# Performance work log

Hardware: AMD Instinct MI355X
Metric: run time of the kernel (lower is better)

The kernel has to match this reference:

```python
import jax, jax.numpy as jnp
import numpy as np

B, S, H, D = 4, 4096, 1024, 64  # batch, seq, hidden_size, kvq_size


def setup_inputs() -> dict:
    key = jax.random.key(0)
    kx, kk, kq, kv = jax.random.split(key, 4)
    scale = 1.0 / np.sqrt(H)  # torch Linear default init range ~ U(-1/sqrt(in), 1/sqrt(in))
    return {
        "x": jax.random.normal(kx, (B, S, H), dtype=jnp.float32),
        "Wk": jax.random.uniform(kk, (H, D), dtype=jnp.float32, minval=-scale, maxval=scale),
        "Wq": jax.random.uniform(kq, (H, D), dtype=jnp.float32, minval=-scale, maxval=scale),
        "Wv": jax.random.uniform(kv, (H, D), dtype=jnp.float32, minval=-scale, maxval=scale),
    }


def reference(x, Wk, Wq, Wv):
    # Projections: [B,S,H] @ [H,D] -> [B,S,D]
    k = jnp.einsum("bsh,hd->bsd", x, Wk)
    q = jnp.einsum("bsh,hd->bsd", x, Wq)
    v = jnp.einsum("bsh,hd->bsd", x, Wv)
    inv_sqrt_d = 1.0 / jnp.sqrt(jnp.asarray(D, dtype=x.dtype))
    # No softmax: attention = Q K^T / sqrt(D), then @ V
    attn = jnp.einsum("bqd,bkd->bqk", q, k) * inv_sqrt_d  # [B,S,S]
    return jnp.einsum("bqk,bkd->bqd", attn, v)  # [B,S,D]
```

## Files before the change

### kernel.cpp

```cpp
#include <hip/hip_runtime.h>
#include <hip/hip_bf16.h>

#define B_ 4
#define S_ 4096
#define H_ 1024
#define D_ 64
#define BK 64
#define KSTEPS (H_ / BK)

typedef short bf16x8 __attribute__((ext_vector_type(8)));
typedef float f32x4 __attribute__((ext_vector_type(4)));

__device__ inline unsigned short f2bf(float f) {
    union { float f; unsigned u; } v; v.f = f;
    return (unsigned short)((v.u + 0x7fffu + ((v.u >> 16) & 1u)) >> 16);
}
__device__ inline float bf2f(unsigned short u) {
    union { unsigned u; float f; } v; v.u = (unsigned)u << 16;
    return v.f;
}
__device__ inline bf16x8 cvt8(const float4& a, const float4& b) {
    bf16x8 r;
    r[0] = (short)f2bf(a.x); r[1] = (short)f2bf(a.y);
    r[2] = (short)f2bf(a.z); r[3] = (short)f2bf(a.w);
    r[4] = (short)f2bf(b.x); r[5] = (short)f2bf(b.y);
    r[6] = (short)f2bf(b.z); r[7] = (short)f2bf(b.w);
    return r;
}

__global__ void prep_w3(const float* __restrict__ Wk, const float* __restrict__ Wv,
                        const float* __restrict__ Wq, unsigned short* __restrict__ WT) {
    int gid = blockIdx.x * 256 + threadIdx.x;
    int d = gid >> 10;
    int h = gid & (H_ - 1);
    WT[gid]           = f2bf(Wk[h * D_ + d]);
    WT[65536 + gid]   = f2bf(Wv[h * D_ + d]);
    WT[131072 + gid]  = f2bf(Wq[h * D_ + d]);
}

__global__ __launch_bounds__(768)
void kv_moment10(const float* __restrict__ x, const unsigned short* __restrict__ WT,
                 unsigned short* __restrict__ pMb, unsigned short* __restrict__ Qb) {
    int blk = blockIdx.x;
    int b = blk >> 6;
    int c = blk & 63;
    int s0 = c * 64;
    int tid = threadIdx.x;
    int w = tid >> 6, lane = tid & 63;
    int r = lane & 15, kg = lane >> 4;
    int sv = w & 3, pj = w >> 2;

    __shared__ __align__(16) unsigned short L[32768];

    int strow = tid >> 3, sts = tid & 7;
    int sf_st = sts ^ (strow & 7);
    int ws0 = tid * 2, ws1 = tid * 2 + 1;
    int wpj0 = ws0 >> 9, wpj1 = ws1 >> 9;
    int wp0 = ws0 & 511, wp1 = ws1 & 511;
    int wrow0 = wp0 >> 3, wst0 = wp0 & 7, wsf0 = wst0 ^ (wrow0 & 7);
    int wrow1 = wp1 >> 3, wst1 = wp1 & 7, wsf1 = wst1 ^ (wrow1 & 7);

    const float* xbase = x + ((size_t)b * S_ + s0) * H_;

    float4 xr0, xr1;
    bf16x8 wr0, wr1;

#define LOADX(KS) do { if (tid < 512) {                                       \
        const float* src = xbase + (size_t)strow * H_ + (KS) * BK + sts * 8;  \
        xr0 = *(const float4*)(src);                                          \
        xr1 = *(const float4*)(src + 4); } } while (0)
#define LOADW(KS) do {                                                        \
        wr0 = *(const bf16x8*)(WT + wpj0 * 65536 + wrow0 * H_ + (KS) * BK + wst0 * 8); \
        wr1 = *(const bf16x8*)(WT + wpj1 * 65536 + wrow1 * H_ + (KS) * BK + wst1 * 8); \
    } while (0)
#define WRITE(BUF) do {                                                       \
        if (tid < 512)                                                        \
            *(bf16x8*)&L[(BUF) * 4096 + strow * 64 + sf_st * 8] = cvt8(xr0, xr1); \
        *(bf16x8*)&L[8192 + (wpj0 * 2 + (BUF)) * 4096 + wrow0 * 64 + wsf0 * 8] = wr0; \
        *(bf16x8*)&L[8192 + (wpj1 * 2 + (BUF)) * 4096 + wrow1 * 64 + wsf1 * 8] = wr1; \
    } while (0)

    LOADX(0); LOADW(0);
    WRITE(0);
    LOADX(1); LOADW(1);
    __syncthreads();

    f32x4 acc[4] = {};
    int arow_off = (sv * 16 + r) * 64;

    for (int ks = 0; ks < KSTEPS; ++ks) {
        int cur = ks & 1;
        if (ks < KSTEPS - 1) WRITE(cur ^ 1);
        if (ks < KSTEPS - 2) { LOADX(ks + 2); LOADW(ks + 2); }
#pragma unroll
        for (int kc = 0; kc < 2; ++kc) {
            int slot = kc * 4 + kg;
            int sf = (slot ^ (r & 7)) * 8;
            bf16x8 af = *(const bf16x8*)&L[cur * 4096 + arow_off + sf];
#pragma unroll
            for (int nt = 0; nt < 4; ++nt) {
                bf16x8 bw = *(const bf16x8*)&L[8192 + (pj * 2 + cur) * 4096 + (nt * 16 + r) * 64 + sf];
                acc[nt] = __builtin_amdgcn_mfma_f32_16x16x32_bf16(af, bw, acc[nt], 0, 0, 0);
            }
        }
        __syncthreads();
    }

    if (pj < 2) {
#pragma unroll
        for (int nt = 0; nt < 4; ++nt)
#pragma unroll
            for (int i = 0; i < 4; ++i)
                L[pj * 4096 + (sv * 16 + kg * 4 + i) * 64 + nt * 16 + r] = f2bf(acc[nt][i]);
    }
    __syncthreads();
    if (pj == 2) {
        unsigned short* qrow = Qb + ((size_t)b * S_ + s0 + sv * 16) * 64;
#pragma unroll
        for (int nt = 0; nt < 4; ++nt)
#pragma unroll
            for (int i = 0; i < 4; ++i)
                qrow[(kg * 4 + i) * 64 + nt * 16 + r] = f2bf(acc[nt][i]);
    } else if (w < 8) {
        int et = w & 3, dh2 = w >> 2;
        f32x4 accM[2] = {};
#pragma unroll
        for (int ks2 = 0; ks2 < 2; ++ks2) {
            bf16x8 afm;
#pragma unroll
            for (int i = 0; i < 8; ++i)
                afm[i] = (short)L[(ks2 * 32 + kg * 8 + i) * 64 + et * 16 + r];
#pragma unroll
            for (int t = 0; t < 2; ++t) {
                int nt = dh2 * 2 + t;
                bf16x8 bfv;
#pragma unroll
                for (int i = 0; i < 8; ++i)
                    bfv[i] = (short)L[4096 + (ks2 * 32 + kg * 8 + i) * 64 + nt * 16 + r];
                accM[t] = __builtin_amdgcn_mfma_f32_16x16x32_bf16(afm, bfv, accM[t], 0, 0, 0);
            }
        }
#pragma unroll
        for (int t = 0; t < 2; ++t)
#pragma unroll
            for (int i = 0; i < 4; ++i) {
                int idx = (et * 16 + kg * 4 + i) * 64 + (dh2 * 2 + t) * 16 + r;
                pMb[((size_t)b * 4096 + idx) * 64 + c] = f2bf(accM[t][i]);
            }
    }
#undef LOADX
#undef LOADW
#undef WRITE
}

__global__ void reduce_m8(const unsigned short* __restrict__ pMb, float* __restrict__ M8) {
    int gid = blockIdx.x * 256 + threadIdx.x;
    const unsigned short* p = pMb + (size_t)gid * 64;
    float s = 0.f;
#pragma unroll
    for (int j = 0; j < 8; ++j) {
        bf16x8 v = *(const bf16x8*)(p + j * 8);
#pragma unroll
        for (int e = 0; e < 8; ++e) s += bf2f((unsigned short)v[e]);
    }
    M8[gid] = s * 0.125f;
}

__global__ __launch_bounds__(256)
void final_qm(const unsigned short* __restrict__ Qb, const float* __restrict__ M8,
              float* __restrict__ out) {
    int blk = blockIdx.x;
    int b = blk >> 6;
    int s0 = (blk & 63) * 64;
    int tid = threadIdx.x;
    int wv = tid >> 6, lane = tid & 63;
    int r = lane & 15, kg = lane >> 4;

    __shared__ unsigned short Ml[4096];
#pragma unroll
    for (int j = 0; j < 16; ++j) {
        int i2 = j * 256 + tid;
        Ml[i2] = f2bf(M8[b * 4096 + i2]);
    }
    __syncthreads();

    const unsigned short* qrow = Qb + ((size_t)b * S_ + s0 + wv * 16 + r) * 64;
    f32x4 acc[4] = {};
#pragma unroll
    for (int ks2 = 0; ks2 < 2; ++ks2) {
        bf16x8 af = *(const bf16x8*)(qrow + ks2 * 32 + kg * 8);
#pragma unroll
        for (int nt = 0; nt < 4; ++nt) {
            bf16x8 bfm;
#pragma unroll
            for (int i = 0; i < 8; ++i)
                bfm[i] = (short)Ml[(ks2 * 32 + kg * 8 + i) * 64 + nt * 16 + r];
            acc[nt] = __builtin_amdgcn_mfma_f32_16x16x32_bf16(af, bfm, acc[nt], 0, 0, 0);
        }
    }
    float* orow = out + ((size_t)b * S_ + s0 + wv * 16) * 64;
#pragma unroll
    for (int nt = 0; nt < 4; ++nt)
#pragma unroll
        for (int i = 0; i < 4; ++i)
            orow[(kg * 4 + i) * 64 + nt * 16 + r] = acc[nt][i];
}

extern "C" void kernel_launch(void* const* d_in, const int* in_sizes, int n_in,
                              void* d_out, int out_size, void* d_ws, size_t ws_size,
                              hipStream_t stream) {
    const float* x  = (const float*)d_in[0];
    const float* Wk = (const float*)d_in[1];
    const float* Wq = (const float*)d_in[2];
    const float* Wv = (const float*)d_in[3];
    float* out = (float*)d_out;

    if (ws_size < 4653056) return;

    char* ws = (char*)d_ws;
    unsigned short* WT  = (unsigned short*)(ws);
    float* M8           = (float*)(ws + 393216);
    unsigned short* Qb  = (unsigned short*)(ws + 458752);
    unsigned short* pMb = (unsigned short*)(ws + 2555904);

    prep_w3<<<256, 256, 0, stream>>>(Wk, Wv, Wq, WT);
    kv_moment10<<<256, 768, 0, stream>>>(x, WT, pMb, Qb);
    reduce_m8<<<64, 256, 0, stream>>>(pMb, M8);
    final_qm<<<256, 256, 0, stream>>>(Qb, M8, out);
}
```

Before: 37.53 us.

## Pre-swizzle weights into LDS tile layout and load via global_load_lds

The weight prep kernel now writes the bf16 transposed weights already in the per-k-step, XOR-swizzled LDS tile layout. The main projection kernel streams each 8 KB weight tile straight from global memory into LDS with the direct global-to-LDS load builtin, dropping the register staging and ds_write for weights. This frees registers and VALU/LDS-write work, but the async LDS write must be visible before the barrier, and the per-step pipeline now has only one-step lookahead for weights.

```diff
diff --git a/kernel.cpp b/kernel.cpp
--- a/kernel.cpp
+++ b/kernel.cpp
@@ -28,18 +28,27 @@
     return r;
 }
 
+__device__ inline void gl_lds16(const unsigned short* g, unsigned short* l) {
+    __builtin_amdgcn_global_load_lds(
+        (const __attribute__((address_space(1))) unsigned int*)g,
+        (__attribute__((address_space(3))) unsigned int*)l,
+        16, 0, 0);
+}
+
 __global__ void prep_w3(const float* __restrict__ Wk, const float* __restrict__ Wv,
-                        const float* __restrict__ Wq, unsigned short* __restrict__ WT) {
+                        const float* __restrict__ Wq, unsigned short* __restrict__ WTs) {
     int gid = blockIdx.x * 256 + threadIdx.x;
-    int d = gid >> 10;
-    int h = gid & (H_ - 1);
-    WT[gid]           = f2bf(Wk[h * D_ + d]);
-    WT[65536 + gid]   = f2bf(Wv[h * D_ + d]);
-    WT[131072 + gid]  = f2bf(Wq[h * D_ + d]);
+    int pj = gid >> 16;
+    int d = (gid >> 10) & 63;
+    int h = gid & 1023;
+    const float* W = (pj == 0) ? Wk : (pj == 1) ? Wv : Wq;
+    int ks = h >> 6, s = (h >> 3) & 7, j = h & 7;
+    int sf = s ^ (d & 7);
+    WTs[((pj * 16 + ks) * 64 + d) * 64 + sf * 8 + j] = f2bf(W[h * 64 + d]);
 }
 
 __global__ __launch_bounds__(768)
-void kv_moment10(const float* __restrict__ x, const unsigned short* __restrict__ WT,
+void kv_moment11(const float* __restrict__ x, const unsigned short* __restrict__ WTs,
                  unsigned short* __restrict__ pMb, unsigned short* __restrict__ Qb) {
     int blk = blockIdx.x;
     int b = blk >> 6;
@@ -54,35 +63,32 @@
 
     int strow = tid >> 3, sts = tid & 7;
     int sf_st = sts ^ (strow & 7);
-    int ws0 = tid * 2, ws1 = tid * 2 + 1;
-    int wpj0 = ws0 >> 9, wpj1 = ws1 >> 9;
-    int wp0 = ws0 & 511, wp1 = ws1 & 511;
-    int wrow0 = wp0 >> 3, wst0 = wp0 & 7, wsf0 = wst0 ^ (wrow0 & 7);
-    int wrow1 = wp1 >> 3, wst1 = wp1 & 7, wsf1 = wst1 ^ (wrow1 & 7);
+    int ci0 = w * 2, ci1 = w * 2 + 1;
+    int cpj0 = ci0 >> 3, cch0 = ci0 & 7;
+    int cpj1 = ci1 >> 3, cch1 = ci1 & 7;
 
     const float* xbase = x + ((size_t)b * S_ + s0) * H_;
 
     float4 xr0, xr1;
-    bf16x8 wr0, wr1;
 
 #define LOADX(KS) do { if (tid < 512) {                                       \
         const float* src = xbase + (size_t)strow * H_ + (KS) * BK + sts * 8;  \
         xr0 = *(const float4*)(src);                                          \
         xr1 = *(const float4*)(src + 4); } } while (0)
-#define LOADW(KS) do {                                                        \
-        wr0 = *(const bf16x8*)(WT + wpj0 * 65536 + wrow0 * H_ + (KS) * BK + wst0 * 8); \
-        wr1 = *(const bf16x8*)(WT + wpj1 * 65536 + wrow1 * H_ + (KS) * BK + wst1 * 8); \
+#define WRITEX(BUF) do { if (tid < 512)                                       \
+        *(bf16x8*)&L[(BUF) * 4096 + strow * 64 + sf_st * 8] = cvt8(xr0, xr1); \
     } while (0)
-#define WRITE(BUF) do {                                                       \
-        if (tid < 512)                                                        \
-            *(bf16x8*)&L[(BUF) * 4096 + strow * 64 + sf_st * 8] = cvt8(xr0, xr1); \
-        *(bf16x8*)&L[8192 + (wpj0 * 2 + (BUF)) * 4096 + wrow0 * 64 + wsf0 * 8] = wr0; \
-        *(bf16x8*)&L[8192 + (wpj1 * 2 + (BUF)) * 4096 + wrow1 * 64 + wsf1 * 8] = wr1; \
+#define GLLDSW(BUF, KS) do {                                                  \
+        gl_lds16(WTs + ((cpj0 * 16 + (KS)) * 4096) + cch0 * 512 + lane * 8,   \
+                 &L[8192 + (cpj0 * 2 + (BUF)) * 4096 + cch0 * 512]);          \
+        gl_lds16(WTs + ((cpj1 * 16 + (KS)) * 4096) + cch1 * 512 + lane * 8,   \
+                 &L[8192 + (cpj1 * 2 + (BUF)) * 4096 + cch1 * 512]);          \
     } while (0)
 
-    LOADX(0); LOADW(0);
-    WRITE(0);
-    LOADX(1); LOADW(1);
+    GLLDSW(0, 0);
+    LOADX(0);
+    WRITEX(0);
+    LOADX(1);
     __syncthreads();
 
     f32x4 acc[4] = {};
@@ -90,8 +96,11 @@
 
     for (int ks = 0; ks < KSTEPS; ++ks) {
         int cur = ks & 1;
-        if (ks < KSTEPS - 1) WRITE(cur ^ 1);
-        if (ks < KSTEPS - 2) { LOADX(ks + 2); LOADW(ks + 2); }
+        if (ks < KSTEPS - 1) {
+            GLLDSW(cur ^ 1, ks + 1);
+            WRITEX(cur ^ 1);
+        }
+        if (ks < KSTEPS - 2) LOADX(ks + 2);
 #pragma unroll
         for (int kc = 0; kc < 2; ++kc) {
             int slot = kc * 4 + kg;
@@ -149,8 +158,8 @@
             }
     }
 #undef LOADX
-#undef LOADW
-#undef WRITE
+#undef WRITEX
+#undef GLLDSW
 }
 
 __global__ void reduce_m8(const unsigned short* __restrict__ pMb, float* __restrict__ M8) {
@@ -218,13 +227,13 @@
     if (ws_size < 4653056) return;
 
     char* ws = (char*)d_ws;
-    unsigned short* WT  = (unsigned short*)(ws);
+    unsigned short* WTs = (unsigned short*)(ws);
     float* M8           = (float*)(ws + 393216);
     unsigned short* Qb  = (unsigned short*)(ws + 458752);
     unsigned short* pMb = (unsigned short*)(ws + 2555904);
 
-    prep_w3<<<256, 256, 0, stream>>>(Wk, Wv, Wq, WT);
-    kv_moment10<<<256, 768, 0, stream>>>(x, WT, pMb, Qb);
+    prep_w3<<<768, 256, 0, stream>>>(Wk, Wv, Wq, WTs);
+    kv_moment11<<<256, 768, 0, stream>>>(x, WTs, pMb, Qb);
     reduce_m8<<<64, 256, 0, stream>>>(pMb, M8);
     final_qm<<<256, 256, 0, stream>>>(Qb, M8, out);
 }
```

Result: slower. 38.77 us (+3.3%).
